# Optimization experiments

Measured on AMD Instinct MI355X. Metric: run time of the kernel, lower is better.

## Reference

```python
import jax, jax.numpy as jnp
import numpy as np

NUM_HEADS = 16

def _apply_rope(t, cos, sin):
    # t: [B, nh, S, hd]; cos/sin: [S, hd//2]
    t1 = t[..., 0::2]
    t2 = t[..., 1::2]
    c = cos[None, None, :, :]
    s = sin[None, None, :, :]
    r1 = t1 * c - t2 * s
    r2 = t1 * s + t2 * c
    # interleave back to [..., hd]
    out = jnp.stack([r1, r2], axis=-1)
    return out.reshape(t.shape)

def setup_inputs() -> dict:
    key = jax.random.key(0)
    ks = jax.random.split(key, 6)
    B, S, H = 1, 4096, 1024
    hd = H // NUM_HEADS
    x = jax.random.normal(ks[0], (B, S, H), dtype=jnp.float32)
    # RoPE angle matrix: theta[pos, i] = pos / 10000^(2i/hd), shape [context, hd//2]
    pos = jnp.arange(S, dtype=jnp.float32)[:, None]
    inv_freq = 1.0 / (10000.0 ** (jnp.arange(0, hd, 2, dtype=jnp.float32) / hd))
    rotation = pos * inv_freq[None, :]
    sc = 1.0 / np.sqrt(H)
    W_qkv = jax.random.normal(ks[1], (H, 3 * H), dtype=jnp.float32) * sc
    b_qkv = jax.random.normal(ks[2], (3 * H,), dtype=jnp.float32) * 0.01
    W_out = jax.random.normal(ks[3], (H, H), dtype=jnp.float32) * sc
    b_out = jax.random.normal(ks[4], (H,), dtype=jnp.float32) * 0.01
    return {"x": x, "rotation": rotation, "W_qkv": W_qkv, "b_qkv": b_qkv,
            "W_out": W_out, "b_out": b_out, "window_size": 33}

def reference(x, rotation, W_qkv, b_qkv, W_out, b_out, window_size):
    B, S, H = x.shape
    nh = NUM_HEADS
    hd = H // nh
    W = window_size
    pad = W // 2
    qkv = x @ W_qkv + b_qkv                               # [B, S, 3H]
    qkv = qkv.reshape(B, S, nh, 3 * hd).transpose(0, 2, 1, 3)  # [B, nh, S, 3hd]
    q, k, v = jnp.split(qkv, 3, axis=-1)                  # each [B, nh, S, hd]
    cos = jnp.cos(rotation[:S])
    sin = jnp.sin(rotation[:S])
    q = _apply_rope(q, cos, sin)
    k = _apply_rope(k, cos, sin)
    # zero-pad along sequence, then gather sliding windows
    k_pad = jnp.pad(k, ((0, 0), (0, 0), (pad, pad), (0, 0)))
    v_pad = jnp.pad(v, ((0, 0), (0, 0), (pad, pad), (0, 0)))
    idx = jnp.arange(S)[:, None] + jnp.arange(W)[None, :]  # [S, W]
    k_win = k_pad[:, :, idx, :]                            # [B, nh, S, W, hd]
    v_win = v_pad[:, :, idx, :]
    scores = jnp.einsum('bnsh,bnswh->bnsw', q, k_win) / np.sqrt(hd)
    attn = jax.nn.softmax(scores, axis=-1)
    ctx = jnp.einsum('bnsw,bnswh->bnsh', attn, v_win)      # [B, nh, S, hd]
    ctx = ctx.transpose(0, 2, 1, 3).reshape(B, S, H)
    return ctx @ W_out + b_out
```

## Files before the change

kernel.cpp:

```cpp
#include <hip/hip_runtime.h>
#include <hip/hip_bf16.h>

#define S_LEN 4096
#define NH 16
#define HD 64
#define WIN 33
#define PAD 16
#define QT 64
#define KROWS 96
#define KPITCH_U 36

#define BM 128
#define BN 128
#define BK 64

typedef short short8 __attribute__((ext_vector_type(8)));
typedef float f32x4 __attribute__((ext_vector_type(4)));

__device__ __forceinline__ float bl(unsigned u){ return __uint_as_float(u << 16); }
__device__ __forceinline__ float bh(unsigned u){ return __uint_as_float(u & 0xffff0000u); }
__device__ __forceinline__ unsigned f2bfu(float f){
  unsigned u = __float_as_uint(f);
  return (u + 0x7fffu + ((u >> 16) & 1u)) >> 16;
}
__device__ __forceinline__ unsigned pack2(float a, float b){ return f2bfu(a) | (f2bfu(b) << 16); }

__device__ __forceinline__ void gload_lds16(const void* g, void* l){
  __builtin_amdgcn_global_load_lds(
      (const __attribute__((address_space(1))) void*)g,
      (__attribute__((address_space(3))) void*)l, 16, 0, 0);
}


__global__ __launch_bounds__(256) void prep_all(
    const float* __restrict__ rot, float2* __restrict__ csq,
    const float* __restrict__ x, __hip_bfloat16* __restrict__ xb,
    const float* __restrict__ Wq, __hip_bfloat16* __restrict__ Wt1,
    const float* __restrict__ Wo, __hip_bfloat16* __restrict__ Wt2)
{
  __shared__ float tile[32][33];
  const int b = blockIdx.x, tid = threadIdx.x;
  if (b < 512) {
    int t = b * 256 + tid;
    float v = rot[t], sv, cv;
    __sincosf(v, &sv, &cv);
    csq[t] = make_float2(cv, sv);
  } else if (b < 2560) {
    int t = (b - 512) * 256 + tid;
    const float4* p = (const float4*)x + (size_t)t * 2;
    float4 a = p[0], c = p[1];
    uint4 o;
    o.x = pack2(a.x, a.y); o.y = pack2(a.z, a.w);
    o.z = pack2(c.x, c.y); o.w = pack2(c.z, c.w);
    ((uint4*)xb)[t] = o;
  } else {
    const float* in; unsigned short* out; int R, C, bx, by;
    if (b < 5632) { int bb = b - 2560; in = Wq; out = (unsigned short*)Wt1; R = 1024; C = 3072; bx = bb % 96; by = bb / 96; }
    else          { int bb = b - 5632; in = Wo; out = (unsigned short*)Wt2; R = 1024; C = 1024; bx = bb % 32; by = bb / 32; }
    int c0 = bx * 32, r0 = by * 32;
    int tx = tid & 31, ty = tid >> 5;
    #pragma unroll
    for (int i = 0; i < 4; ++i) {
      int r = ty + i * 8;
      tile[r][tx] = in[(size_t)(r0 + r) * C + c0 + tx];
    }
    __syncthreads();
    #pragma unroll
    for (int i = 0; i < 4; ++i) {
      int cc = ty + i * 8;
      out[(size_t)(c0 + cc) * R + r0 + tx] = (unsigned short)f2bfu(tile[tx][cc]);
    }
  }
}


__global__ __launch_bounds__(256) void gemm_qkv_rope(
    const __hip_bfloat16* __restrict__ A,
    const __hip_bfloat16* __restrict__ Bt,
    const float* __restrict__ bias,
    const float2* __restrict__ csq,
    unsigned short* __restrict__ Cout,
    int M, int N, int K)
{
  __shared__ unsigned int lA[2][BM * BK / 2];
  __shared__ unsigned int lB[2][BN * BK / 2];
  const int tid = threadIdx.x;
  const int wave = tid >> 6, lane = tid & 63;
  const int flat = blockIdx.y * 24 + blockIdx.x;
  const int swz = (flat & 7) * 96 + (flat >> 3);
  const int m0 = (swz / 24) * BM, n0 = (swz % 24) * BN;
  const int wm = (wave >> 1) * 64, wn = (wave & 1) * 64;
  const int l16 = lane >> 4, l15 = lane & 15;

  f32x4 acc[4][4];
  #pragma unroll
  for (int i = 0; i < 4; ++i)
    #pragma unroll
    for (int j = 0; j < 4; ++j) acc[i][j] = (f32x4){0.f, 0.f, 0.f, 0.f};

  auto stage = [&](int buf, int kt) {
    #pragma unroll
    for (int it = 0; it < 4; ++it) {
      const int c = it * 256 + wave * 64 + lane;
      const int r = c >> 3, s8 = c & 7;
      const int ss = s8 ^ (r & 7);
      gload_lds16(A  + (size_t)(m0 + r) * K + kt * BK + ss * 8,
                  (char*)lA[buf] + (it * 256 + wave * 64) * 16);
      gload_lds16(Bt + (size_t)(n0 + r) * K + kt * BK + ss * 8,
                  (char*)lB[buf] + (it * 256 + wave * 64) * 16);
    }
  };

  const int nkt = K / BK;
  stage(0, 0);
  __syncthreads();
  int cur = 0;
  for (int kt = 0; kt < nkt; ++kt) {
    if (kt + 1 < nkt) stage(cur ^ 1, kt + 1);
    #pragma unroll
    for (int ks = 0; ks < 2; ++ks) {
      short8 af[4], bfr[4];
      #pragma unroll
      for (int mi = 0; mi < 4; ++mi) {
        const int r = wm + mi * 16 + l15;
        const int slot = (ks * 4 + l16) ^ (r & 7);
        uint4 u = *(const uint4*)((const char*)lA[cur] + r * 128 + slot * 16);
        af[mi] = __builtin_bit_cast(short8, u);
      }
      #pragma unroll
      for (int ni = 0; ni < 4; ++ni) {
        const int r = wn + ni * 16 + l15;
        const int slot = (ks * 4 + l16) ^ (r & 7);
        uint4 u = *(const uint4*)((const char*)lB[cur] + r * 128 + slot * 16);
        bfr[ni] = __builtin_bit_cast(short8, u);
      }
      __builtin_amdgcn_s_setprio(1);
      #pragma unroll
      for (int mi = 0; mi < 4; ++mi)
        #pragma unroll
        for (int ni = 0; ni < 4; ++ni)
          acc[mi][ni] = __builtin_amdgcn_mfma_f32_16x16x32_bf16(af[mi], bfr[ni], acc[mi][ni], 0, 0, 0);
      __builtin_amdgcn_s_setprio(0);
    }
    __syncthreads();
    cur ^= 1;
  }

  #pragma unroll
  for (int ni = 0; ni < 4; ++ni) {
    const int cn = n0 + wn + ni * 16 + l15;
    const int rseg = cn % 192;
    const float bv = bias[cn];
    if (rseg < 128) {
      const int i = (rseg & 63) >> 1;
      const float sgn = (cn & 1) ? 1.f : -1.f;
      #pragma unroll
      for (int mi = 0; mi < 4; ++mi) {
        #pragma unroll
        for (int j = 0; j < 4; ++j) {
          const int rm = m0 + wm + mi * 16 + l16 * 4 + j;
          const float v = acc[mi][ni][j] + bv;
          const float p = __shfl_xor(v, 1);
          const float2 cs = csq[rm * 32 + i];
          Cout[(size_t)rm * N + cn] = (unsigned short)f2bfu(v * cs.x + p * (sgn * cs.y));
        }
      }
    } else {
      #pragma unroll
      for (int mi = 0; mi < 4; ++mi) {
        #pragma unroll
        for (int j = 0; j < 4; ++j) {
          const int rm = m0 + wm + mi * 16 + l16 * 4 + j;
          Cout[(size_t)rm * N + cn] = (unsigned short)f2bfu(acc[mi][ni][j] + bv);
        }
      }
    }
  }
}


__global__ __launch_bounds__(256) void gemm_out(
    const __hip_bfloat16* __restrict__ A,
    const __hip_bfloat16* __restrict__ Bt,
    const float* __restrict__ bias,
    float* __restrict__ Cout,
    int M, int N, int K)
{
  __shared__ unsigned int lA[2][128 * 64 / 2];
  __shared__ unsigned int lB[2][64 * 64 / 2];
  const int tid = threadIdx.x;
  const int wave = tid >> 6, lane = tid & 63;
  const int flat = blockIdx.y * 16 + blockIdx.x;
  const int swz = (flat & 7) * 64 + (flat >> 3);
  const int m0 = (swz >> 4) * 128, n0 = (swz & 15) * 64;
  const int wm = (wave >> 1) * 64, wn = (wave & 1) * 32;
  const int l16 = lane >> 4, l15 = lane & 15;

  f32x4 acc[4][2];
  #pragma unroll
  for (int i = 0; i < 4; ++i)
    #pragma unroll
    for (int j = 0; j < 2; ++j) acc[i][j] = (f32x4){0.f, 0.f, 0.f, 0.f};

  auto stage = [&](int buf, int kt) {
    #pragma unroll
    for (int it = 0; it < 4; ++it) {
      const int c = it * 256 + wave * 64 + lane;
      const int r = c >> 3, s8 = c & 7;
      const int ss = s8 ^ (r & 7);
      gload_lds16(A + (size_t)(m0 + r) * K + kt * 64 + ss * 8,
                  (char*)lA[buf] + (it * 256 + wave * 64) * 16);
    }
    #pragma unroll
    for (int it = 0; it < 2; ++it) {
      const int c = it * 256 + wave * 64 + lane;
      const int r = c >> 3, s8 = c & 7;
      const int ss = s8 ^ (r & 7);
      gload_lds16(Bt + (size_t)(n0 + r) * K + kt * 64 + ss * 8,
                  (char*)lB[buf] + (it * 256 + wave * 64) * 16);
    }
  };

  const int nkt = K / 64;
  stage(0, 0);
  __syncthreads();
  int cur = 0;
  for (int kt = 0; kt < nkt; ++kt) {
    if (kt + 1 < nkt) stage(cur ^ 1, kt + 1);
    #pragma unroll
    for (int ks = 0; ks < 2; ++ks) {
      short8 af[4], bfr[2];
      #pragma unroll
      for (int mi = 0; mi < 4; ++mi) {
        const int r = wm + mi * 16 + l15;
        const int slot = (ks * 4 + l16) ^ (r & 7);
        uint4 u = *(const uint4*)((const char*)lA[cur] + r * 128 + slot * 16);
        af[mi] = __builtin_bit_cast(short8, u);
      }
      #pragma unroll
      for (int ni = 0; ni < 2; ++ni) {
        const int r = wn + ni * 16 + l15;
        const int slot = (ks * 4 + l16) ^ (r & 7);
        uint4 u = *(const uint4*)((const char*)lB[cur] + r * 128 + slot * 16);
        bfr[ni] = __builtin_bit_cast(short8, u);
      }
      __builtin_amdgcn_s_setprio(1);
      #pragma unroll
      for (int mi = 0; mi < 4; ++mi)
        #pragma unroll
        for (int ni = 0; ni < 2; ++ni)
          acc[mi][ni] = __builtin_amdgcn_mfma_f32_16x16x32_bf16(af[mi], bfr[ni], acc[mi][ni], 0, 0, 0);
      __builtin_amdgcn_s_setprio(0);
    }
    __syncthreads();
    cur ^= 1;
  }

  #pragma unroll
  for (int ni = 0; ni < 2; ++ni) {
    const int cn = n0 + wn + ni * 16 + l15;
    const float bv = bias[cn];
    #pragma unroll
    for (int mi = 0; mi < 4; ++mi) {
      #pragma unroll
      for (int j = 0; j < 4; ++j) {
        const int rm = m0 + wm + mi * 16 + l16 * 4 + j;
        Cout[(size_t)rm * N + cn] = acc[mi][ni][j] + bv;
      }
    }
  }
}


__global__ __launch_bounds__(256) void attn_kernel(const __hip_bfloat16* __restrict__ qkv,
                                                   __hip_bfloat16* __restrict__ ctx){
  __shared__ unsigned int kbuf[KROWS * KPITCH_U];
  __shared__ unsigned int vbuf[KROWS * KPITCH_U];
  const int tid = threadIdx.x;
  const int h   = blockIdx.x & 15;
  const int qs0 = (blockIdx.x >> 4) * QT;

  #pragma unroll
  for (int it = 0; it < 3; ++it) {
    int c = tid + it * 256;
    int r = c >> 3, s8 = c & 7;
    int srow = qs0 - PAD + r;
    uint4 kv = make_uint4(0, 0, 0, 0), vv = make_uint4(0, 0, 0, 0);
    if ((unsigned)srow < (unsigned)S_LEN) {
      kv = ((const uint4*)(qkv + (size_t)srow * 3072 + h * 192 + 64))[s8];
      vv = ((const uint4*)(qkv + (size_t)srow * 3072 + h * 192 + 128))[s8];
    }
    *(uint4*)(kbuf + r * KPITCH_U + s8 * 4) = kv;
    *(uint4*)(vbuf + r * KPITCH_U + s8 * 4) = vv;
  }

  const int ql = tid >> 2, t4 = tid & 3;
  const uint4* qp = (const uint4*)(qkv + (size_t)(qs0 + ql) * 3072 + h * 192);
  float qf[64];
  #pragma unroll
  for (int c = 0; c < 8; ++c) {
    uint4 v = qp[c];
    qf[c*8+0] = bl(v.x); qf[c*8+1] = bh(v.x);
    qf[c*8+2] = bl(v.y); qf[c*8+3] = bh(v.y);
    qf[c*8+4] = bl(v.z); qf[c*8+5] = bh(v.z);
    qf[c*8+6] = bl(v.w); qf[c*8+7] = bh(v.w);
  }
  __syncthreads();

  float sc[9];
  #pragma unroll
  for (int j = 0; j < 9; ++j) sc[j] = 0.f;
  float mx = -1e30f;
  #pragma unroll
  for (int j = 0; j < 9; ++j) {
    int w = t4 + 4 * j;
    if (w < WIN) {
      int rw = ql + w;
      const uint4* kp = (const uint4*)(kbuf + rw * KPITCH_U);
      float d = 0.f;
      #pragma unroll
      for (int c = 0; c < 8; ++c) {
        uint4 kv = kp[c];
        d += qf[c*8+0]*bl(kv.x) + qf[c*8+1]*bh(kv.x)
           + qf[c*8+2]*bl(kv.y) + qf[c*8+3]*bh(kv.y)
           + qf[c*8+4]*bl(kv.z) + qf[c*8+5]*bh(kv.z)
           + qf[c*8+6]*bl(kv.w) + qf[c*8+7]*bh(kv.w);
      }
      sc[j] = d * 0.125f;
      mx = fmaxf(mx, sc[j]);
    }
  }
  mx = fmaxf(mx, __shfl_xor(mx, 1));
  mx = fmaxf(mx, __shfl_xor(mx, 2));
  float sum = 0.f;
  #pragma unroll
  for (int j = 0; j < 9; ++j) {
    int w = t4 + 4 * j;
    if (w < WIN) { sc[j] = __expf(sc[j] - mx); sum += sc[j]; }
  }
  sum += __shfl_xor(sum, 1);
  sum += __shfl_xor(sum, 2);
  const float inv = 1.0f / sum;
  #pragma unroll
  for (int j = 0; j < 9; ++j) sc[j] *= inv;

  float accd[16];
  #pragma unroll
  for (int i = 0; i < 16; ++i) accd[i] = 0.f;
  #pragma unroll
  for (int w = 0; w < WIN; ++w) {
    float wgt = __shfl(sc[w >> 2], ((tid & 63) & ~3) | (w & 3), 64);
    int rw = ql + w;
    const uint4* vp = (const uint4*)(vbuf + rw * KPITCH_U + t4 * 8);
    uint4 a = vp[0], b = vp[1];
    float vf[16];
    vf[0]=bl(a.x); vf[1]=bh(a.x); vf[2]=bl(a.y); vf[3]=bh(a.y);
    vf[4]=bl(a.z); vf[5]=bh(a.z); vf[6]=bl(a.w); vf[7]=bh(a.w);
    vf[8]=bl(b.x); vf[9]=bh(b.x); vf[10]=bl(b.y); vf[11]=bh(b.y);
    vf[12]=bl(b.z); vf[13]=bh(b.z); vf[14]=bl(b.w); vf[15]=bh(b.w);
    #pragma unroll
    for (int i = 0; i < 16; ++i) accd[i] += wgt * vf[i];
  }

  unsigned short* op = (unsigned short*)ctx + (size_t)(qs0 + ql) * 1024 + h * 64 + t4 * 16;
  uint4 o1, o2;
  o1.x = pack2(accd[0], accd[1]);  o1.y = pack2(accd[2], accd[3]);
  o1.z = pack2(accd[4], accd[5]);  o1.w = pack2(accd[6], accd[7]);
  o2.x = pack2(accd[8], accd[9]);  o2.y = pack2(accd[10], accd[11]);
  o2.z = pack2(accd[12], accd[13]); o2.w = pack2(accd[14], accd[15]);
  *(uint4*)op = o1;
  *((uint4*)op + 1) = o2;
}


extern "C" void kernel_launch(void* const* d_in, const int* in_sizes, int n_in,
                              void* d_out, int out_size, void* d_ws, size_t ws_size,
                              hipStream_t stream)
{
  const float* x     = (const float*)d_in[0];
  const float* rot   = (const float*)d_in[1];
  const float* W_qkv = (const float*)d_in[2];
  const float* b_qkv = (const float*)d_in[3];
  const float* W_out = (const float*)d_in[4];
  const float* b_out = (const float*)d_in[5];
  float* out = (float*)d_out;

  char* ws = (char*)d_ws;
  __hip_bfloat16* xb   = (__hip_bfloat16*)(ws + 0);
  __hip_bfloat16* Wt1  = (__hip_bfloat16*)(ws + 8388608);
  __hip_bfloat16* Wt2  = (__hip_bfloat16*)(ws + 14680064);
  __hip_bfloat16* qkvb = (__hip_bfloat16*)(ws + 16777216);
  __hip_bfloat16* ctx  = (__hip_bfloat16*)(ws + 41943040);
  float2* csq          = (float2*)(ws + 50331648);

  prep_all<<<6656, 256, 0, stream>>>(rot, csq, x, xb, W_qkv, Wt1, W_out, Wt2);
  gemm_qkv_rope<<<dim3(3072 / BN, 4096 / BM), 256, 0, stream>>>(xb, Wt1, b_qkv, csq,
                                                                (unsigned short*)qkvb, 4096, 3072, 1024);
  attn_kernel<<<64 * 16, 256, 0, stream>>>(qkvb, ctx);
  gemm_out<<<dim3(1024 / 64, 4096 / 128), 256, 0, stream>>>(ctx, Wt2, b_out, out, 4096, 1024, 1024);
}
```

Measured before the change: 95.23 us.

## Use partial vmcnt waits for prefetch overlap and XCD-aware tile mapping in GEMMs

The __syncthreads after each K-tile is replaced with explicit s_waitcnt vmcnt(N) plus s_barrier, so the prefetch of the next tile can stay in flight while the current one is consumed. Previously the full barrier drained every outstanding load, the prefetch included. Block-to-tile mapping is also changed so each XCD gets a contiguous N-column strip and all M rows, which is meant to improve L2 reuse of the weight tiles. The hand-written counts depend on exactly how many global-to-LDS loads are issued per stage, so a miscount could cause races.

```diff
diff --git a/kernel.cpp b/kernel.cpp
--- a/kernel.cpp
+++ b/kernel.cpp
@@ -87,8 +87,9 @@
   const int tid = threadIdx.x;
   const int wave = tid >> 6, lane = tid & 63;
   const int flat = blockIdx.y * 24 + blockIdx.x;
-  const int swz = (flat & 7) * 96 + (flat >> 3);
-  const int m0 = (swz / 24) * BM, n0 = (swz % 24) * BN;
+  const int xcd = flat & 7, local = flat >> 3;
+  const int m0 = (local & 31) * BM;
+  const int n0 = (xcd * 3 + (local >> 5)) * BN;
   const int wm = (wave >> 1) * 64, wn = (wave & 1) * 64;
   const int l16 = lane >> 4, l15 = lane & 15;
 
@@ -113,10 +114,14 @@
 
   const int nkt = K / BK;
   stage(0, 0);
-  __syncthreads();
   int cur = 0;
   for (int kt = 0; kt < nkt; ++kt) {
-    if (kt + 1 < nkt) stage(cur ^ 1, kt + 1);
+    const bool pf = (kt + 1 < nkt);
+    if (pf) stage(cur ^ 1, kt + 1);
+    if (pf) asm volatile("s_waitcnt vmcnt(8)" ::: "memory");
+    else    asm volatile("s_waitcnt vmcnt(0)" ::: "memory");
+    __builtin_amdgcn_s_barrier();
+    __builtin_amdgcn_sched_barrier(0);
     #pragma unroll
     for (int ks = 0; ks < 2; ++ks) {
       short8 af[4], bfr[4];
@@ -142,7 +147,8 @@
           acc[mi][ni] = __builtin_amdgcn_mfma_f32_16x16x32_bf16(af[mi], bfr[ni], acc[mi][ni], 0, 0, 0);
       __builtin_amdgcn_s_setprio(0);
     }
-    __syncthreads();
+    __builtin_amdgcn_sched_barrier(0);
+    __builtin_amdgcn_s_barrier();
     cur ^= 1;
   }
 
@@ -191,8 +197,9 @@
   const int tid = threadIdx.x;
   const int wave = tid >> 6, lane = tid & 63;
   const int flat = blockIdx.y * 16 + blockIdx.x;
-  const int swz = (flat & 7) * 64 + (flat >> 3);
-  const int m0 = (swz >> 4) * 128, n0 = (swz & 15) * 64;
+  const int xcd = flat & 7, local = flat >> 3;
+  const int m0 = (local & 31) * 128;
+  const int n0 = (xcd * 2 + (local >> 5)) * 64;
   const int wm = (wave >> 1) * 64, wn = (wave & 1) * 32;
   const int l16 = lane >> 4, l15 = lane & 15;
 
@@ -223,10 +230,14 @@
 
   const int nkt = K / 64;
   stage(0, 0);
-  __syncthreads();
   int cur = 0;
   for (int kt = 0; kt < nkt; ++kt) {
-    if (kt + 1 < nkt) stage(cur ^ 1, kt + 1);
+    const bool pf = (kt + 1 < nkt);
+    if (pf) stage(cur ^ 1, kt + 1);
+    if (pf) asm volatile("s_waitcnt vmcnt(6)" ::: "memory");
+    else    asm volatile("s_waitcnt vmcnt(0)" ::: "memory");
+    __builtin_amdgcn_s_barrier();
+    __builtin_amdgcn_sched_barrier(0);
     #pragma unroll
     for (int ks = 0; ks < 2; ++ks) {
       short8 af[4], bfr[2];
@@ -252,7 +263,8 @@
           acc[mi][ni] = __builtin_amdgcn_mfma_f32_16x16x32_bf16(af[mi], bfr[ni], acc[mi][ni], 0, 0, 0);
       __builtin_amdgcn_s_setprio(0);
     }
-    __syncthreads();
+    __builtin_amdgcn_sched_barrier(0);
+    __builtin_amdgcn_s_barrier();
     cur ^= 1;
   }
 
```

Result: no change. 96.98 us (+1.8%).
